# Kernel optimization log

Measured on AMD Instinct MI355X. Metric: run time of the kernel, lower is better.

Reference implementation:

```python
import jax, jax.numpy as jnp
import numpy as np

B, S, D, H = 2, 2048, 1024, 16
DH = D // H
EPS = 1e-5
NEG = -1e9


def _layer_norm(x, g, b):
    m = jnp.mean(x, axis=-1, keepdims=True)
    v = jnp.mean(jnp.square(x - m), axis=-1, keepdims=True)
    return (x - m) * jax.lax.rsqrt(v + EPS) * g + b


def setup_inputs() -> dict:
    key = jax.random.key(0)
    ks = jax.random.split(key, 10)
    std = 0.02
    inp = {
        "x": jax.random.normal(ks[0], (B, S, D), dtype=jnp.float32),
        "src_mask": jax.random.randint(ks[1], (B, S), 0, 2) > 0,
        # projection weights stored as (in, out) so y = x @ w + b
        "wq": jax.random.normal(ks[2], (D, D), dtype=jnp.float32) * std,
        "bq": jnp.zeros((D,), jnp.float32),
        "wk": jax.random.normal(ks[3], (D, D), dtype=jnp.float32) * std,
        "bk": jnp.zeros((D,), jnp.float32),
        "wv": jax.random.normal(ks[4], (D, D), dtype=jnp.float32) * std,
        "bv": jnp.zeros((D,), jnp.float32),
        "wo": jax.random.normal(ks[5], (D, D), dtype=jnp.float32) * std,
        "bo": jnp.zeros((D,), jnp.float32),
        "ln1_g": jnp.ones((D,), jnp.float32),
        "ln1_b": jnp.zeros((D,), jnp.float32),
        "w1": jax.random.normal(ks[6], (D, 2 * D), dtype=jnp.float32) * std,
        "b1": jnp.zeros((2 * D,), jnp.float32),
        "w2": jax.random.normal(ks[7], (2 * D, D), dtype=jnp.float32) * std,
        "b2": jnp.zeros((D,), jnp.float32),
        "ln2_g": jnp.ones((D,), jnp.float32),
        "ln2_b": jnp.zeros((D,), jnp.float32),
    }
    return inp


def reference(x, src_mask, wq, bq, wk, bk, wv, bv, wo, bo,
              ln1_g, ln1_b, w1, b1, w2, b2, ln2_g, ln2_b):
    b, s, d = x.shape
    # Q/K/V projections, split into heads: [B, S, H, DH]
    q = (x @ wq + bq).reshape(b, s, H, DH)
    k = (x @ wk + bk).reshape(b, s, H, DH)
    v = (x @ wv + bv).reshape(b, s, H, DH)
    # scaled scores [B, H, Sq, Sk] (matches torch's split/cat over heads)
    scores = jnp.einsum('bqhd,bkhd->bhqk', q, k) / jnp.sqrt(jnp.float32(DH))
    # additive key mask: -1e9 where src_mask is False
    scores = scores + jnp.where(src_mask, 0.0, NEG)[:, None, None, :]
    A = jax.nn.softmax(scores, axis=-1)
    attn = jnp.einsum('bhqk,bkhd->bqhd', A, v).reshape(b, s, d)
    attn_out = attn @ wo + bo + x
    h = _layer_norm(attn_out, ln1_g, ln1_b)
    ffn = jax.nn.relu(h @ w1 + b1) @ w2 + b2
    return _layer_norm(ffn + h, ln2_g, ln2_b)
```

## Files before the change

kernel.cpp:

```cpp
#include <hip/hip_runtime.h>
#include <math.h>

#define BB  2
#define SS  2048
#define DD  1024
#define HH  16
#define DHH 64
#define MM  (BB * SS)

typedef float f32x4 __attribute__((ext_vector_type(4)));
typedef short s16x8 __attribute__((ext_vector_type(8)));

__device__ __forceinline__ unsigned short f2b(float f) {
    union { float f; unsigned u; } v; v.f = f;
    unsigned r = v.u + 0x7fffu + ((v.u >> 16) & 1u);
    return (unsigned short)(r >> 16);
}
__device__ __forceinline__ float b2f(unsigned short u) {
    union { unsigned u; float f; } v; v.u = ((unsigned)u) << 16;
    return v.f;
}
__device__ __forceinline__ unsigned cvtpk(float lo, float hi) {
    unsigned r;
    asm("v_cvt_pk_bf16_f32 %0, %1, %2" : "=v"(r) : "v"(lo), "v"(hi));
    return r;
}

typedef __attribute__((address_space(1))) void gv_t;
typedef __attribute__((address_space(3))) void lv_t;
__device__ __forceinline__ void gld16(const void* g, void* l) {
    __builtin_amdgcn_global_load_lds((gv_t*)(void*)g, (lv_t*)l, 16, 0, 0);
}

__device__ __forceinline__ int sigma(int row) { return (row + (row >> 3)) & 7; }
__device__ __forceinline__ int sidx(int row, int col) {
    return row * 64 + (col ^ (sigma(row) << 3));
}

template <int RELU, int RES, int OUTF, int VS>
__global__ __launch_bounds__(256)
void mgemm(const unsigned short* __restrict__ A, const unsigned short* __restrict__ B,
           const float* __restrict__ bias, const void* __restrict__ res,
           void* __restrict__ out, unsigned short* __restrict__ vt,
           int M, int N, int K, int outN)
{
    __shared__ short As[128 * 64];
    __shared__ short Bs[128 * 64];

    const int tid  = threadIdx.x;
    const int wave = tid >> 6, lane = tid & 63;

    const int nwg = gridDim.x * gridDim.y;
    const int bid = blockIdx.y * gridDim.x + blockIdx.x;
    const int swz = (bid & 7) * (nwg >> 3) + (bid >> 3);
    const int by = swz / gridDim.x;
    const int bx = swz - by * gridDim.x;
    const int bm = by * 128, bn = bx * 128;

    const int srow = tid >> 3;
    const int scol = (tid & 7) * 8;
    const int wr = wave >> 1, wc = wave & 1;
    const int fr = lane & 15;
    const int fk = (lane >> 4) * 8;

    f32x4 acc[4][4];
#pragma unroll
    for (int i = 0; i < 4; ++i)
#pragma unroll
        for (int j = 0; j < 4; ++j) acc[i][j] = (f32x4){0.f, 0.f, 0.f, 0.f};

    for (int k0 = 0; k0 < K; k0 += 64) {
#pragma unroll
        for (int it = 0; it < 4; ++it) {
            gld16(&A[(size_t)(bm + it * 32 + srow) * K + k0 + scol],
                  &As[it * 2048 + wave * 512]);
            gld16(&B[(size_t)(bn + it * 32 + srow) * K + k0 + scol],
                  &Bs[it * 2048 + wave * 512]);
        }
        __syncthreads();

#pragma unroll
        for (int kk = 0; kk < 2; ++kk) {
            s16x8 af[4], bf[4];
#pragma unroll
            for (int i = 0; i < 4; ++i)
                af[i] = *(const s16x8*)&As[(wr * 64 + i * 16 + fr) * 64 + kk * 32 + fk];
#pragma unroll
            for (int j = 0; j < 4; ++j)
                bf[j] = *(const s16x8*)&Bs[(wc * 64 + j * 16 + fr) * 64 + kk * 32 + fk];
#pragma unroll
            for (int i = 0; i < 4; ++i)
#pragma unroll
                for (int j = 0; j < 4; ++j)
                    acc[i][j] = __builtin_amdgcn_mfma_f32_16x16x32_bf16(
                        af[i], bf[j], acc[i][j], 0, 0, 0);
        }
        __syncthreads();
    }

    const int r0 = bm + wr * 64 + (lane >> 4) * 4;
    const int c0 = bn + wc * 64 + (lane & 15);
    const float* resf          = (const float*)res;
    const unsigned short* resh = (const unsigned short*)res;
    float* outf          = (float*)out;
    unsigned short* outh = (unsigned short*)out;

    if (VS == 1 && bn >= 2048) {
#pragma unroll
        for (int i = 0; i < 4; ++i)
#pragma unroll
            for (int j = 0; j < 4; ++j) {
                const int col = c0 + j * 16;
                const int hh = (col >> 6) & 15, dh = col & 63;
                const float bcol = bias[col];
#pragma unroll
                for (int r = 0; r < 4; ++r) {
                    const int row = r0 + i * 16 + r;
                    const int bb = row >> 11, s = row & 2047;
                    vt[(size_t)(((bb * 16 + hh) * 64) + dh) * 2048 + s] =
                        f2b(acc[i][j][r] + bcol);
                }
            }
        return;
    }

#pragma unroll
    for (int i = 0; i < 4; ++i)
#pragma unroll
        for (int j = 0; j < 4; ++j) {
            const int col = c0 + j * 16;
            const float bcol = bias[col];
#pragma unroll
            for (int r = 0; r < 4; ++r) {
                const int row = r0 + i * 16 + r;
                float v = acc[i][j][r] + bcol;
                if (RES == 1) v += resf[(size_t)row * outN + col];
                if (RES == 2) v += b2f(resh[(size_t)row * outN + col]);
                if (RELU)     v = fmaxf(v, 0.f);
                if (OUTF) outf[(size_t)row * outN + col] = v;
                else      outh[(size_t)row * outN + col] = f2b(v);
            }
        }
}

__global__ __launch_bounds__(256)
void prep(const float* __restrict__ x,
          const float* __restrict__ wq, const float* __restrict__ wk,
          const float* __restrict__ wv, const float* __restrict__ wo,
          const float* __restrict__ w1, const float* __restrict__ w2,
          const float* __restrict__ bq, const float* __restrict__ bk,
          const float* __restrict__ bv,
          unsigned short* __restrict__ xb, unsigned short* __restrict__ wqkvT,
          unsigned short* __restrict__ woT, unsigned short* __restrict__ w1T,
          unsigned short* __restrict__ w2T, float* __restrict__ bqkv)
{
    __shared__ float T[64][65];
    const int tid = threadIdx.x;
    int bid = blockIdx.x;

    if (bid < 4096) {
        const int i = bid * 256 + tid;
        const float4 v = ((const float4*)x)[i];
        ushort4 o4;
        o4.x = f2b(v.x); o4.y = f2b(v.y); o4.z = f2b(v.z); o4.w = f2b(v.w);
        ((ushort4*)xb)[i] = o4;
        return;
    }
    bid -= 4096;

    if (bid >= 2048) {
        const int i = (bid - 2048) * 256 + tid;
        if (i < 1024) bqkv[i] = bq[i];
        else if (i < 2048) bqkv[i] = bk[i - 1024];
        else if (i < 3072) bqkv[i] = bv[i - 2048];
        return;
    }

    const float* src; unsigned short* dst; int K, N, nbx, sub;
    if (bid < 256)       { src = wq; dst = wqkvT;               K = 1024; N = 1024; nbx = 16; sub = bid; }
    else if (bid < 512)  { src = wk; dst = wqkvT + 1024 * 1024; K = 1024; N = 1024; nbx = 16; sub = bid - 256; }
    else if (bid < 768)  { src = wv; dst = wqkvT + 2048 * 1024; K = 1024; N = 1024; nbx = 16; sub = bid - 512; }
    else if (bid < 1024) { src = wo; dst = woT;                 K = 1024; N = 1024; nbx = 16; sub = bid - 768; }
    else if (bid < 1536) { src = w1; dst = w1T;                 K = 1024; N = 2048; nbx = 32; sub = bid - 1024; }
    else                 { src = w2; dst = w2T;                 K = 2048; N = 1024; nbx = 16; sub = bid - 1536; }

    const int n0 = (sub % nbx) * 64, k0 = (sub / nbx) * 64;
    const int c = tid & 63, rb = tid >> 6;
#pragma unroll
    for (int it = 0; it < 16; ++it) {
        const int r = it * 4 + rb;
        T[r][c] = src[(size_t)(k0 + r) * N + n0 + c];
    }
    __syncthreads();
#pragma unroll
    for (int it = 0; it < 16; ++it) {
        const int r = it * 4 + rb;
        dst[(size_t)(n0 + r) * K + k0 + c] = f2b(T[c][r]);
    }
}

__global__ __launch_bounds__(512)
void attn_mfma(const unsigned short* __restrict__ qk,
               const unsigned short* __restrict__ vt,
               const int* __restrict__ mask, unsigned short* __restrict__ o)
{
    const int b = blockIdx.z, h = blockIdx.y, q0 = blockIdx.x * 128;
    __shared__ unsigned short QP[8192];
    __shared__ unsigned short Ks[4096];
    __shared__ unsigned short Vs[4096];
    __shared__ float maskf[64];
    const int tid = threadIdx.x, wave = tid >> 6, lane = tid & 63;
    const int grp = lane >> 4, l16 = lane & 15;

    const size_t qkbase = (size_t)(b * SS) * 2048 + h * DHH;
    const size_t vbase  = (size_t)((b * HH + h) * 64) * 2048;
    const float SC = 0.18033688f;
    const float MNEG = -1.442695e9f;

#pragma unroll
    for (int it = 0; it < 2; ++it) {
        const int slot = it * 512 + tid;
        const int row = slot >> 3, dhb = slot & 7;
        const int src = (dhb ^ sigma(row)) * 8;
        gld16(&qk[qkbase + (size_t)(q0 + row) * 2048 + src],
              &QP[it * 4096 + wave * 512]);
    }
    const int krow = tid >> 3, kdhb = tid & 7;
    const int ksrc = (kdhb ^ sigma(krow)) * 8;
    __syncthreads();
    const int prow = wave * 16 + l16;
    const s16x8 aq0 = *(const s16x8*)&QP[sidx(prow, grp * 8)];
    const s16x8 aq1 = *(const s16x8*)&QP[sidx(prow, 32 + grp * 8)];

    const s16x8 ones = {(short)0x3F80, (short)0x3F80, (short)0x3F80, (short)0x3F80,
                        (short)0x3F80, (short)0x3F80, (short)0x3F80, (short)0x3F80};

    f32x4 accO[4];
#pragma unroll
    for (int j = 0; j < 4; ++j) accO[j] = (f32x4){0.f, 0.f, 0.f, 0.f};
    f32x4 accS = (f32x4){0.f, 0.f, 0.f, 0.f};
    float mrow = -1e30f;

    for (int kt = 0; kt < SS / 64; ++kt) {
        const int kv0 = kt * 64;
        __syncthreads();
        gld16(&qk[qkbase + (size_t)(kv0 + krow) * 2048 + 1024 + ksrc], &Ks[wave * 512]);
        gld16(&vt[vbase + (size_t)krow * 2048 + kv0 + ksrc],           &Vs[wave * 512]);
        if (tid < 64) maskf[tid] = mask[b * SS + kv0 + tid] ? 0.f : MNEG;
        __syncthreads();

        f32x4 sv[4];
        __builtin_amdgcn_s_setprio(1);
#pragma unroll
        for (int j = 0; j < 4; ++j) {
            const s16x8 bk0 = *(const s16x8*)&Ks[sidx(j * 16 + l16, grp * 8)];
            const s16x8 bk1 = *(const s16x8*)&Ks[sidx(j * 16 + l16, 32 + grp * 8)];
            f32x4 z = (f32x4){0.f, 0.f, 0.f, 0.f};
            z = __builtin_amdgcn_mfma_f32_16x16x32_bf16(bk0, aq0, z, 0, 0, 0);
            z = __builtin_amdgcn_mfma_f32_16x16x32_bf16(bk1, aq1, z, 0, 0, 0);
            sv[j] = z;
        }
        __builtin_amdgcn_s_setprio(0);
#pragma unroll
        for (int j = 0; j < 4; ++j) {
            const float4 mv = *(const float4*)&maskf[j * 16 + grp * 4];
            sv[j][0] = sv[j][0] * SC + mv.x;
            sv[j][1] = sv[j][1] * SC + mv.y;
            sv[j][2] = sv[j][2] * SC + mv.z;
            sv[j][3] = sv[j][3] * SC + mv.w;
        }

        float mx = -1e30f;
#pragma unroll
        for (int j = 0; j < 4; ++j)
#pragma unroll
            for (int r = 0; r < 4; ++r) mx = fmaxf(mx, sv[j][r]);
        mx = fmaxf(mx, __shfl_xor(mx, 16));
        mx = fmaxf(mx, __shfl_xor(mx, 32));

        if (!__all(mx <= mrow + 8.f)) {
            const float mnew = fmaxf(mrow, mx);
            const float corrq = __builtin_amdgcn_exp2f(mrow - mnew);
            mrow = mnew;
            float cr[4];
#pragma unroll
            for (int r = 0; r < 4; ++r) cr[r] = __shfl(corrq, grp * 4 + r);
#pragma unroll
            for (int r = 0; r < 4; ++r) {
                accS[r] *= cr[r];
#pragma unroll
                for (int j = 0; j < 4; ++j) accO[j][r] *= cr[r];
            }
        }

#pragma unroll
        for (int j = 0; j < 4; ++j) {
            const float p0 = __builtin_amdgcn_exp2f(sv[j][0] - mrow);
            const float p1 = __builtin_amdgcn_exp2f(sv[j][1] - mrow);
            const float p2 = __builtin_amdgcn_exp2f(sv[j][2] - mrow);
            const float p3 = __builtin_amdgcn_exp2f(sv[j][3] - mrow);
            *(unsigned*)&QP[sidx(prow, j * 16 + grp * 4)]     = cvtpk(p0, p1);
            *(unsigned*)&QP[sidx(prow, j * 16 + grp * 4 + 2)] = cvtpk(p2, p3);
        }

        const s16x8 pa0 = *(const s16x8*)&QP[sidx(prow, grp * 8)];
        const s16x8 pa1 = *(const s16x8*)&QP[sidx(prow, 32 + grp * 8)];
        __builtin_amdgcn_s_setprio(1);
        accS = __builtin_amdgcn_mfma_f32_16x16x32_bf16(pa0, ones, accS, 0, 0, 0);
        accS = __builtin_amdgcn_mfma_f32_16x16x32_bf16(pa1, ones, accS, 0, 0, 0);
#pragma unroll
        for (int j = 0; j < 4; ++j) {
            const s16x8 vb0 = *(const s16x8*)&Vs[sidx(j * 16 + l16, grp * 8)];
            const s16x8 vb1 = *(const s16x8*)&Vs[sidx(j * 16 + l16, 32 + grp * 8)];
            accO[j] = __builtin_amdgcn_mfma_f32_16x16x32_bf16(pa0, vb0, accO[j], 0, 0, 0);
            accO[j] = __builtin_amdgcn_mfma_f32_16x16x32_bf16(pa1, vb1, accO[j], 0, 0, 0);
        }
        __builtin_amdgcn_s_setprio(0);
    }

#pragma unroll
    for (int r = 0; r < 4; ++r) {
        const float inv = 1.0f / accS[r];
        const int row = q0 + wave * 16 + grp * 4 + r;
#pragma unroll
        for (int j = 0; j < 4; ++j)
            o[(size_t)(b * SS + row) * DD + h * DHH + j * 16 + l16] =
                f2b(accO[j][r] * inv);
    }
}

template <int OUTBF>
__global__ __launch_bounds__(256)
void ln_kernel(const float* __restrict__ x, const float* __restrict__ g,
               const float* __restrict__ beta, void* __restrict__ outv)
{
    const int row = blockIdx.x;
    const int tid = threadIdx.x;
    const float4 xl = reinterpret_cast<const float4*>(x + (size_t)row * DD)[tid];
    float s  = xl.x + xl.y + xl.z + xl.w;
    float sq = xl.x * xl.x + xl.y * xl.y + xl.z * xl.z + xl.w * xl.w;
#pragma unroll
    for (int off = 1; off < 64; off <<= 1) {
        s  += __shfl_xor(s, off);
        sq += __shfl_xor(sq, off);
    }
    __shared__ float ssum[4], ssq[4];
    const int wid = tid >> 6;
    if ((tid & 63) == 0) { ssum[wid] = s; ssq[wid] = sq; }
    __syncthreads();
    s  = ssum[0] + ssum[1] + ssum[2] + ssum[3];
    sq = ssq[0]  + ssq[1]  + ssq[2]  + ssq[3];
    const float mean = s * (1.0f / DD);
    const float var  = fmaxf(sq * (1.0f / DD) - mean * mean, 0.0f);
    const float rstd = rsqrtf(var + 1e-5f);
    const float4 gv = reinterpret_cast<const float4*>(g)[tid];
    const float4 bv = reinterpret_cast<const float4*>(beta)[tid];
    float4 ov;
    ov.x = (xl.x - mean) * rstd * gv.x + bv.x;
    ov.y = (xl.y - mean) * rstd * gv.y + bv.y;
    ov.z = (xl.z - mean) * rstd * gv.z + bv.z;
    ov.w = (xl.w - mean) * rstd * gv.w + bv.w;
    if (OUTBF) {
        ushort4 o4;
        o4.x = f2b(ov.x); o4.y = f2b(ov.y); o4.z = f2b(ov.z); o4.w = f2b(ov.w);
        reinterpret_cast<ushort4*>(outv)[(size_t)row * 256 + tid] = o4;
    } else {
        reinterpret_cast<float4*>(outv)[(size_t)row * 256 + tid] = ov;
    }
}

extern "C" void kernel_launch(void* const* d_in, const int* in_sizes, int n_in,
                              void* d_out, int out_size, void* d_ws, size_t ws_size,
                              hipStream_t stream)
{
    (void)in_sizes; (void)n_in; (void)out_size; (void)ws_size;

    const float* x     = (const float*)d_in[0];
    const int*   mask  = (const int*)  d_in[1];
    const float* wq    = (const float*)d_in[2];
    const float* bq    = (const float*)d_in[3];
    const float* wk    = (const float*)d_in[4];
    const float* bk    = (const float*)d_in[5];
    const float* wv    = (const float*)d_in[6];
    const float* bv    = (const float*)d_in[7];
    const float* wo    = (const float*)d_in[8];
    const float* bo    = (const float*)d_in[9];
    const float* ln1_g = (const float*)d_in[10];
    const float* ln1_b = (const float*)d_in[11];
    const float* w1    = (const float*)d_in[12];
    const float* b1    = (const float*)d_in[13];
    const float* w2    = (const float*)d_in[14];
    const float* b2    = (const float*)d_in[15];
    const float* ln2_g = (const float*)d_in[16];
    const float* ln2_b = (const float*)d_in[17];

    float* out = (float*)d_out;
    char*  wsb = (char*)d_ws;
    const size_t MB = 1u << 20;

    unsigned short* wqkvT = (unsigned short*)(wsb + 0);
    unsigned short* woT   = (unsigned short*)(wsb + 6 * MB);
    unsigned short* w1T   = (unsigned short*)(wsb + 8 * MB);
    unsigned short* w2T   = (unsigned short*)(wsb + 12 * MB);
    float*          bqkv  = (float*)(wsb + 16 * MB);
    unsigned short* qkb   = (unsigned short*)(wsb + 17 * MB);
    unsigned short* vtb   = (unsigned short*)(wsb + 33 * MB);
    unsigned short* xb    = (unsigned short*)(wsb + 41 * MB);
    unsigned short* ab16  = xb;
    float*          t0    = (float*)(wsb + 17 * MB);
    unsigned short* hb16  = (unsigned short*)(wsb + 33 * MB);
    unsigned short* f1b   = (unsigned short*)(wsb + 41 * MB);
    float*          t1    = (float*)(wsb + 17 * MB);

    prep<<<6156, 256, 0, stream>>>(x, wq, wk, wv, wo, w1, w2, bq, bk, bv,
                                   xb, wqkvT, woT, w1T, w2T, bqkv);
    mgemm<0, 0, 0, 1><<<dim3(24, 32), 256, 0, stream>>>(
        xb, wqkvT, bqkv, nullptr, qkb, vtb, MM, 3 * DD, DD, 2048);
    attn_mfma<<<dim3(SS / 128, HH, BB), 512, 0, stream>>>(qkb, vtb, mask, ab16);
    mgemm<0, 1, 1, 0><<<dim3(8, 32), 256, 0, stream>>>(
        ab16, woT, bo, x, t0, nullptr, MM, DD, DD, DD);
    ln_kernel<1><<<MM, 256, 0, stream>>>(t0, ln1_g, ln1_b, hb16);
    mgemm<1, 0, 0, 0><<<dim3(16, 32), 256, 0, stream>>>(
        hb16, w1T, b1, nullptr, f1b, nullptr, MM, 2 * DD, DD, 2 * DD);
    mgemm<0, 2, 1, 0><<<dim3(8, 32), 256, 0, stream>>>(
        f1b, w2T, b2, hb16, t1, nullptr, MM, DD, 2 * DD, DD);
    ln_kernel<0><<<MM, 256, 0, stream>>>(t1, ln2_g, ln2_b, out);
}
```

Baseline: 246.4 us.

## Use 128x64 GEMM tiles for N=1024 GEMMs, bf16 intermediates, drop block swizzle

Adds a BN template parameter so the two N=1024 GEMMs (output projection and FFN down-projection) use 128x64 tiles and launch 512 workgroups instead of 256, which fills the CUs better. Their pre-layernorm outputs are now stored as bf16 instead of fp32, and layernorm reads bf16 input, which cuts memory traffic. The workgroup swizzle for L2 locality is removed from every GEMM. Storing the residual sums in bf16 before layernorm loses precision, and dropping the swizzle may hurt cache reuse.

```diff
diff --git a/kernel.cpp b/kernel.cpp
--- a/kernel.cpp
+++ b/kernel.cpp
@@ -37,7 +37,7 @@
     return row * 64 + (col ^ (sigma(row) << 3));
 }
 
-template <int RELU, int RES, int OUTF, int VS>
+template <int RELU, int RES, int OUTF, int VS, int BN>
 __global__ __launch_bounds__(256)
 void mgemm(const unsigned short* __restrict__ A, const unsigned short* __restrict__ B,
            const float* __restrict__ bias, const void* __restrict__ res,
@@ -45,51 +45,47 @@
            int M, int N, int K, int outN)
 {
     __shared__ short As[128 * 64];
-    __shared__ short Bs[128 * 64];
+    __shared__ short Bs[BN * 64];
 
     const int tid  = threadIdx.x;
     const int wave = tid >> 6, lane = tid & 63;
-
-    const int nwg = gridDim.x * gridDim.y;
-    const int bid = blockIdx.y * gridDim.x + blockIdx.x;
-    const int swz = (bid & 7) * (nwg >> 3) + (bid >> 3);
-    const int by = swz / gridDim.x;
-    const int bx = swz - by * gridDim.x;
-    const int bm = by * 128, bn = bx * 128;
-
+    const int bm = blockIdx.y * 128, bn = blockIdx.x * BN;
     const int srow = tid >> 3;
     const int scol = (tid & 7) * 8;
-    const int wr = wave >> 1, wc = wave & 1;
     const int fr = lane & 15;
     const int fk = (lane >> 4) * 8;
-
-    f32x4 acc[4][4];
-#pragma unroll
-    for (int i = 0; i < 4; ++i)
+    const int wrow = (BN == 128) ? (wave >> 1) * 64 : wave * 32;
+    const int wcol = (BN == 128) ? (wave & 1) * 64 : 0;
+    constexpr int MI = (BN == 128) ? 4 : 2;
+
+    f32x4 acc[MI][4];
+#pragma unroll
+    for (int i = 0; i < MI; ++i)
 #pragma unroll
         for (int j = 0; j < 4; ++j) acc[i][j] = (f32x4){0.f, 0.f, 0.f, 0.f};
 
     for (int k0 = 0; k0 < K; k0 += 64) {
 #pragma unroll
-        for (int it = 0; it < 4; ++it) {
+        for (int it = 0; it < 4; ++it)
             gld16(&A[(size_t)(bm + it * 32 + srow) * K + k0 + scol],
                   &As[it * 2048 + wave * 512]);
+#pragma unroll
+        for (int it = 0; it < BN / 32; ++it)
             gld16(&B[(size_t)(bn + it * 32 + srow) * K + k0 + scol],
                   &Bs[it * 2048 + wave * 512]);
-        }
         __syncthreads();
 
 #pragma unroll
         for (int kk = 0; kk < 2; ++kk) {
-            s16x8 af[4], bf[4];
-#pragma unroll
-            for (int i = 0; i < 4; ++i)
-                af[i] = *(const s16x8*)&As[(wr * 64 + i * 16 + fr) * 64 + kk * 32 + fk];
+            s16x8 af[MI], bf[4];
+#pragma unroll
+            for (int i = 0; i < MI; ++i)
+                af[i] = *(const s16x8*)&As[(wrow + i * 16 + fr) * 64 + kk * 32 + fk];
 #pragma unroll
             for (int j = 0; j < 4; ++j)
-                bf[j] = *(const s16x8*)&Bs[(wc * 64 + j * 16 + fr) * 64 + kk * 32 + fk];
-#pragma unroll
-            for (int i = 0; i < 4; ++i)
+                bf[j] = *(const s16x8*)&Bs[(wcol + j * 16 + fr) * 64 + kk * 32 + fk];
+#pragma unroll
+            for (int i = 0; i < MI; ++i)
 #pragma unroll
                 for (int j = 0; j < 4; ++j)
                     acc[i][j] = __builtin_amdgcn_mfma_f32_16x16x32_bf16(
@@ -98,8 +94,8 @@
         __syncthreads();
     }
 
-    const int r0 = bm + wr * 64 + (lane >> 4) * 4;
-    const int c0 = bn + wc * 64 + (lane & 15);
+    const int r0 = bm + wrow + (lane >> 4) * 4;
+    const int c0 = bn + wcol + (lane & 15);
     const float* resf          = (const float*)res;
     const unsigned short* resh = (const unsigned short*)res;
     float* outf          = (float*)out;
@@ -107,7 +103,7 @@
 
     if (VS == 1 && bn >= 2048) {
 #pragma unroll
-        for (int i = 0; i < 4; ++i)
+        for (int i = 0; i < MI; ++i)
 #pragma unroll
             for (int j = 0; j < 4; ++j) {
                 const int col = c0 + j * 16;
@@ -125,7 +121,7 @@
     }
 
 #pragma unroll
-    for (int i = 0; i < 4; ++i)
+    for (int i = 0; i < MI; ++i)
 #pragma unroll
         for (int j = 0; j < 4; ++j) {
             const int col = c0 + j * 16;
@@ -329,16 +325,23 @@
     }
 }
 
-template <int OUTBF>
+template <int INBF, int OUTBF>
 __global__ __launch_bounds__(256)
-void ln_kernel(const float* __restrict__ x, const float* __restrict__ g,
+void ln_kernel(const void* __restrict__ xv, const float* __restrict__ g,
                const float* __restrict__ beta, void* __restrict__ outv)
 {
     const int row = blockIdx.x;
     const int tid = threadIdx.x;
-    const float4 xl = reinterpret_cast<const float4*>(x + (size_t)row * DD)[tid];
-    float s  = xl.x + xl.y + xl.z + xl.w;
-    float sq = xl.x * xl.x + xl.y * xl.y + xl.z * xl.z + xl.w * xl.w;
+    float x0, x1, x2, x3;
+    if (INBF) {
+        const ushort4 xi = reinterpret_cast<const ushort4*>(xv)[(size_t)row * 256 + tid];
+        x0 = b2f(xi.x); x1 = b2f(xi.y); x2 = b2f(xi.z); x3 = b2f(xi.w);
+    } else {
+        const float4 xi = reinterpret_cast<const float4*>(xv)[(size_t)row * 256 + tid];
+        x0 = xi.x; x1 = xi.y; x2 = xi.z; x3 = xi.w;
+    }
+    float s  = x0 + x1 + x2 + x3;
+    float sq = x0 * x0 + x1 * x1 + x2 * x2 + x3 * x3;
 #pragma unroll
     for (int off = 1; off < 64; off <<= 1) {
         s  += __shfl_xor(s, off);
@@ -356,10 +359,10 @@
     const float4 gv = reinterpret_cast<const float4*>(g)[tid];
     const float4 bv = reinterpret_cast<const float4*>(beta)[tid];
     float4 ov;
-    ov.x = (xl.x - mean) * rstd * gv.x + bv.x;
-    ov.y = (xl.y - mean) * rstd * gv.y + bv.y;
-    ov.z = (xl.z - mean) * rstd * gv.z + bv.z;
-    ov.w = (xl.w - mean) * rstd * gv.w + bv.w;
+    ov.x = (x0 - mean) * rstd * gv.x + bv.x;
+    ov.y = (x1 - mean) * rstd * gv.y + bv.y;
+    ov.z = (x2 - mean) * rstd * gv.z + bv.z;
+    ov.w = (x3 - mean) * rstd * gv.w + bv.w;
     if (OUTBF) {
         ushort4 o4;
         o4.x = f2b(ov.x); o4.y = f2b(ov.y); o4.z = f2b(ov.z); o4.w = f2b(ov.w);
@@ -407,22 +410,22 @@
     unsigned short* vtb   = (unsigned short*)(wsb + 33 * MB);
     unsigned short* xb    = (unsigned short*)(wsb + 41 * MB);
     unsigned short* ab16  = xb;
-    float*          t0    = (float*)(wsb + 17 * MB);
+    unsigned short* t0    = (unsigned short*)(wsb + 17 * MB);
     unsigned short* hb16  = (unsigned short*)(wsb + 33 * MB);
     unsigned short* f1b   = (unsigned short*)(wsb + 41 * MB);
-    float*          t1    = (float*)(wsb + 17 * MB);
+    unsigned short* t1    = (unsigned short*)(wsb + 17 * MB);
 
     prep<<<6156, 256, 0, stream>>>(x, wq, wk, wv, wo, w1, w2, bq, bk, bv,
                                    xb, wqkvT, woT, w1T, w2T, bqkv);
-    mgemm<0, 0, 0, 1><<<dim3(24, 32), 256, 0, stream>>>(
+    mgemm<0, 0, 0, 1, 128><<<dim3(24, 32), 256, 0, stream>>>(
         xb, wqkvT, bqkv, nullptr, qkb, vtb, MM, 3 * DD, DD, 2048);
     attn_mfma<<<dim3(SS / 128, HH, BB), 512, 0, stream>>>(qkb, vtb, mask, ab16);
-    mgemm<0, 1, 1, 0><<<dim3(8, 32), 256, 0, stream>>>(
+    mgemm<0, 1, 0, 0, 64><<<dim3(16, 32), 256, 0, stream>>>(
         ab16, woT, bo, x, t0, nullptr, MM, DD, DD, DD);
-    ln_kernel<1><<<MM, 256, 0, stream>>>(t0, ln1_g, ln1_b, hb16);
-    mgemm<1, 0, 0, 0><<<dim3(16, 32), 256, 0, stream>>>(
+    ln_kernel<1, 1><<<MM, 256, 0, stream>>>(t0, ln1_g, ln1_b, hb16);
+    mgemm<1, 0, 0, 0, 128><<<dim3(16, 32), 256, 0, stream>>>(
         hb16, w1T, b1, nullptr, f1b, nullptr, MM, 2 * DD, DD, 2 * DD);
-    mgemm<0, 2, 1, 0><<<dim3(8, 32), 256, 0, stream>>>(
+    mgemm<0, 2, 0, 0, 64><<<dim3(16, 32), 256, 0, stream>>>(
         f1b, w2T, b2, hb16, t1, nullptr, MM, DD, 2 * DD, DD);
-    ln_kernel<0><<<MM, 256, 0, stream>>>(t1, ln2_g, ln2_b, out);
-}
+    ln_kernel<1, 0><<<MM, 256, 0, stream>>>(t1, ln2_g, ln2_b, out);
+}
```

New measurement: 231.3 us. 1.07x faster.
